# Kernel optimization log

Measured on AMD Instinct MI355X. Metric: run time of the kernel, lower is better.

Reference implementation:

```python
import jax, jax.numpy as jnp
import numpy as np

N_SRC, N_DST, MAX_NEIGH, H = 65536, 8192, 32, 128


def setup_inputs() -> dict:
    key = jax.random.key(0)
    ks = jax.random.split(key, 16)
    inp = {
        'x': jax.random.randint(ks[0], (N_SRC, 2), 0, 1000, dtype=jnp.int64)
             if jax.config.jax_enable_x64 else jax.random.randint(ks[0], (N_SRC, 2), 0, 1000, dtype=jnp.int32),
        'neigh_sim': jax.random.randint(ks[1], (N_DST, MAX_NEIGH), 0, N_SRC, dtype=jnp.int32),
        'neigh_cor': jax.random.randint(ks[2], (N_DST, MAX_NEIGH), 0, N_SRC, dtype=jnp.int32),
        'emb0_sim': jax.random.normal(ks[3], (1000, 32), jnp.float32) * 0.1,
        'emb1_sim': jax.random.normal(ks[4], (100000, 96), jnp.float32) * 0.1,
        'emb0_cor': jax.random.normal(ks[5], (1000, 32), jnp.float32) * 0.1,
        'emb1_cor': jax.random.normal(ks[6], (100000, 96), jnp.float32) * 0.1,
        'W_in_sim': jax.random.normal(ks[7], (H, H), jnp.float32) * 0.05,
        'b_in_sim': jnp.zeros((H,), jnp.float32),
        'W_in_cor': jax.random.normal(ks[8], (H, H), jnp.float32) * 0.05,
        'b_in_cor': jnp.zeros((H,), jnp.float32),
        'W_out_sim': jax.random.normal(ks[9], (H, H), jnp.float32) * 0.05,
        'b_out_sim': jnp.zeros((H,), jnp.float32),
        'W_out_cor': jax.random.normal(ks[10], (H, H), jnp.float32) * 0.05,
        'b_out_cor': jnp.zeros((H,), jnp.float32),
        'W_sim2cor': jax.random.normal(ks[11], (H, H), jnp.float32) * 0.05,
        'W_cor2sim': jax.random.normal(ks[12], (H, H), jnp.float32) * 0.05,
    }
    return inp


def _coattention_pool(D, Q):
    # D, Q: [N, m, H]
    n, m, h = Q.shape
    L = jnp.einsum('nmh,nkh->nmk', D, Q)           # [N, m, m]
    AC = jax.nn.softmax(L, axis=-1)
    AS = jax.nn.softmax(jnp.swapaxes(L, 1, 2), axis=-1)
    CQ = jnp.einsum('nmk,nkh->nmh', AC, Q)          # [N, m, H]
    CD = jnp.einsum('nkm,nmh->nkh', AS, jnp.concatenate([D, CQ], axis=-1))  # [N, m, 2H]
    out = jnp.concatenate([Q, CD], axis=-1)         # [N, m, 3H]
    # AvgPool1d(kernel=3, stride=3) over channel dim, then mean over neighbors
    pooled = out.reshape(n, m, h, 3).mean(axis=-1)  # consecutive triples
    return pooled.mean(axis=1)                       # [N, H]


def _mode_forward(x, neigh_sim, neigh_cor, emb0, emb1, W_in, b_in, W_out, b_out, mode):
    feat = jnp.concatenate([emb0[x[:, 0]], emb1[x[:, 1]]], axis=-1)  # [N_src, 128]
    feat = feat @ W_in + b_in                                        # [N_src, H]
    h_self = feat[: neigh_sim.shape[0]]
    nf_sim = feat[neigh_sim]  # [N_dst, m, H]
    nf_cor = feat[neigh_cor]
    if mode == 'cor':
        D, Q = nf_sim, nf_cor
    else:
        D, Q = nf_cor, nf_sim
    rst = h_self + _coattention_pool(D, Q)
    return rst @ W_out + b_out


def reference(x, neigh_sim, neigh_cor, emb0_sim, emb1_sim, emb0_cor, emb1_cor,
              W_in_sim, b_in_sim, W_in_cor, b_in_cor,
              W_out_sim, b_out_sim, W_out_cor, b_out_cor,
              W_sim2cor, W_cor2sim):
    sim = _mode_forward(x, neigh_sim, neigh_cor, emb0_sim, emb1_sim,
                        W_in_sim, b_in_sim, W_out_sim, b_out_sim, 'sim')
    cor = _mode_forward(x, neigh_sim, neigh_cor, emb0_cor, emb1_cor,
                        W_in_cor, b_in_cor, W_out_cor, b_out_cor, 'cor')
    a1, a2, b2 = 0.5, 0.33, 0.33
    z1sim = (1 - a1) * sim + a1 * (cor @ W_cor2sim)
    z1cor = (1 - a1) * cor + a1 * (sim @ W_sim2cor)
    z2sim = (1 - a2 - b2) * sim + a2 * (cor @ W_cor2sim) + b2 * (z1cor @ W_cor2sim)
    z2cor = (1 - a2 - b2) * cor + a2 * (sim @ W_sim2cor) + b2 * (z1sim @ W_sim2cor)
    return z2sim, z2cor
```

## Files before the change

### kernel.cpp

```cpp
#include <hip/hip_runtime.h>
#include <hip/hip_bf16.h>

#define NSRC 65536
#define NDST 8192
#define H 128

#define C_SELF 0.34f
#define C_CROSS 0.495f
#define C_DBL  0.165f

typedef float f32x16 __attribute__((ext_vector_type(16)));
typedef short bf16x8 __attribute__((ext_vector_type(8)));

static __device__ __forceinline__ float b2f(unsigned short u) {
  union { unsigned int i; float f; } v; v.i = ((unsigned int)u) << 16; return v.f;
}
static __device__ __forceinline__ unsigned short f2b(float f) {
  union { float f; unsigned int i; } v; v.f = f;
  unsigned int x = v.i;
  return (unsigned short)((x + 0x7fffu + ((x >> 16) & 1u)) >> 16);
}
static __device__ __forceinline__ void load4bf(const unsigned short* p, float* d) {
  ushort4 u = *(const ushort4*)p;
  d[0] = b2f(u.x); d[1] = b2f(u.y); d[2] = b2f(u.z); d[3] = b2f(u.w);
}

template <int CTRL>
static __device__ __forceinline__ float dpp_mov(float x) {
  return __int_as_float(__builtin_amdgcn_update_dpp(
      0, __float_as_int(x), CTRL, 0xF, 0xF, true));
}
static __device__ __forceinline__ float dpp_sum32_tail(float x) {
  x += dpp_mov<0x111>(x);
  x += dpp_mov<0x112>(x);
  x += dpp_mov<0x114>(x);
  x += dpp_mov<0x118>(x);
  x += dpp_mov<0x142>(x);
  return x;
}
static __device__ __forceinline__ float allred32_sum(float x) {
  x += dpp_mov<0xB1>(x);
  x += dpp_mov<0x4E>(x);
  x += dpp_mov<0x124>(x);
  x += dpp_mov<0x128>(x);
  x += __int_as_float(__builtin_amdgcn_ds_swizzle(__float_as_int(x), 0x401F));
  return x;
}

static __device__ __forceinline__ void load4any(const void* base, size_t idx, int f32flag, float* d) {
  if (f32flag) {
    float4 v = *(const float4*)((const float*)base + idx);
    d[0] = v.x; d[1] = v.y; d[2] = v.z; d[3] = v.w;
  } else {
    load4bf((const unsigned short*)base + idx, d);
  }
}
static __device__ __forceinline__ float load1any(const void* base, size_t idx, int f32flag) {
  return f32flag ? ((const float*)base)[idx] : b2f(((const unsigned short*)base)[idx]);
}

__global__ void detect(const unsigned short* __restrict__ W, const int* __restrict__ x,
                       int* __restrict__ flags) {
  const int l = threadIdx.x;
  int bad = 0;
#pragma unroll
  for (int i = l; i < 128; i += 64) {
    unsigned short u = W[i];
    if (u != 0) {
      int e = (u >> 7) & 0xFF;
      if (e < 90 || e > 128) bad++;
    }
  }
  int nz = (l < 16) ? (x[2 * l + 1] != 0 ? 1 : 0) : 0;
#pragma unroll
  for (int d = 1; d < 64; d <<= 1) {
    bad += __shfl_xor(bad, d);
    nz  += __shfl_xor(nz, d);
  }
  if (l == 0) {
    flags[0] = (bad > 8) ? 1 : 0;
    flags[1] = (nz == 0) ? 1 : 0;
  }
}

__global__ __launch_bounds__(128) void wprep(
    const void* __restrict__ Wsim, const void* __restrict__ Wcor,
    const int* __restrict__ flags,
    unsigned short* __restrict__ WTsim, unsigned short* __restrict__ WTcor)
{
  const int wf = flags[0];
  const int n = blockIdx.x & 127;
  const void* W = (blockIdx.x & 128) ? Wcor : Wsim;
  unsigned short* WT = (blockIdx.x & 128) ? WTcor : WTsim;
  const int k = threadIdx.x;
  WT[n * 128 + k] = f2b(load1any(W, k * 128 + n, wf));
}

__global__ __launch_bounds__(256) void featgemm_mfma(
    const int* __restrict__ x,
    const void* __restrict__ emb0,
    const void* __restrict__ emb1,
    const unsigned short* __restrict__ WT,
    const void* __restrict__ bvec,
    const int* __restrict__ flags,
    unsigned char* __restrict__ feat8,
    unsigned short* __restrict__ feat16)
{
  const int wf  = flags[0];
  const int x64 = flags[1];
  const int t = threadIdx.x;
  const int w = t >> 6, l = t & 63, lane = l & 31, half = l >> 5;
  const int rbase = blockIdx.x * 128 + w * 32;
  const int r = rbase + lane;

  int x0, x1;
  if (x64) { x0 = x[r * 4]; x1 = x[r * 4 + 2]; }
  else     { x0 = x[r * 2]; x1 = x[r * 2 + 1]; }

  bf16x8 afrag[8];
#pragma unroll
  for (int s = 0; s < 8; ++s) {
    float tmp[8];
    if (s < 2) {
      const size_t base = (size_t)x0 * 32 + s * 16 + half * 8;
      load4any(emb0, base, wf, tmp);
      load4any(emb0, base + 4, wf, tmp + 4);
    } else {
      const size_t base = (size_t)x1 * 96 + (s * 16 - 32) + half * 8;
      load4any(emb1, base, wf, tmp);
      load4any(emb1, base + 4, wf, tmp + 4);
    }
    union { bf16x8 v; unsigned short u[8]; } cv;
#pragma unroll
    for (int j = 0; j < 8; ++j) cv.u[j] = f2b(tmp[j]);
    afrag[s] = cv.v;
  }

  const bool do16 = (rbase < NDST);
#pragma unroll
  for (int strip = 0; strip < 4; ++strip) {
    const int n = strip * 32 + lane;
    const unsigned short* wtrow = WT + (size_t)n * 128 + half * 8;
    f32x16 acc = {0,0,0,0,0,0,0,0,0,0,0,0,0,0,0,0};
#pragma unroll
    for (int s = 0; s < 8; ++s) {
      bf16x8 bfrag = *(const bf16x8*)(wtrow + s * 16);
      acc = __builtin_amdgcn_mfma_f32_32x32x16_bf16(afrag[s], bfrag, acc, 0, 0, 0);
    }
    const float bias_n = load1any(bvec, n, wf);
#pragma unroll
    for (int i = 0; i < 16; ++i) {
      const int m = (i & 3) + 8 * (i >> 2) + 4 * half;
      const int row = rbase + m;
      const float val = acc[i] + bias_n;
      const int p8 = __builtin_amdgcn_cvt_pk_fp8_f32(val, val, 0, false);
      feat8[(size_t)row * H + n] = (unsigned char)(p8 & 0xFF);
      if (do16) feat16[(size_t)row * H + n] = f2b(val);
    }
  }
}

__global__ __launch_bounds__(256) void coatt_mfma(
    const unsigned char* __restrict__ feat8,
    const unsigned short* __restrict__ feat16,
    const int* __restrict__ idxD,
    const int* __restrict__ idxQ,
    unsigned short* __restrict__ rst)
{
  __shared__ float gbuf[4][448];
  const int t = threadIdx.x;
  const int w = t >> 6;
  const int l = t & 63;
  const int r = l & 31;
  const int half = l >> 5;
  const int n = blockIdx.x * 4 + w;

  float* g   = gbuf[w];
  float* svb = gbuf[w] + 384;
  float* tvb = gbuf[w] + 416;

  const int gD = idxD[n * 32 + r];
  const int gQ = idxQ[n * 32 + r];
  const unsigned char* drow = feat8 + (size_t)gD * H + half * 8;
  const unsigned char* qrow = feat8 + (size_t)gQ * H + half * 8;

  long dfrag[8], qfrag[8];
#pragma unroll
  for (int s = 0; s < 8; ++s) {
    dfrag[s] = *(const long*)(drow + s * 16);
    qfrag[s] = *(const long*)(qrow + s * 16);
  }

  f32x16 acc = {0,0,0,0,0,0,0,0,0,0,0,0,0,0,0,0};
#pragma unroll
  for (int s = 0; s < 8; ++s)
    acc = __builtin_amdgcn_mfma_f32_32x32x16_fp8_fp8(dfrag[s], qfrag[s], acc, 0, 0, 0);

  float ex[16], rrcp[16];
#pragma unroll
  for (int i = 0; i < 16; ++i) ex[i] = __expf(acc[i]);
#pragma unroll
  for (int i = 0; i < 16; ++i) rrcp[i] = 1.0f / allred32_sum(ex[i]);
  float csum = 0.f;
#pragma unroll
  for (int i = 0; i < 16; ++i) csum += ex[i];
  csum += __shfl_xor(csum, 32);
  const float crcp = 1.0f / csum;

  float svt[16];
#pragma unroll
  for (int i = 0; i < 16; ++i) svt[i] = dpp_sum32_tail(ex[i] * crcp);
  if (r == 31) {
    *(float4*)(svb + 4 * half)      = make_float4(svt[0],  svt[1],  svt[2],  svt[3]);
    *(float4*)(svb + 8 + 4 * half)  = make_float4(svt[4],  svt[5],  svt[6],  svt[7]);
    *(float4*)(svb + 16 + 4 * half) = make_float4(svt[8],  svt[9],  svt[10], svt[11]);
    *(float4*)(svb + 24 + 4 * half) = make_float4(svt[12], svt[13], svt[14], svt[15]);
  }
  float sv16[16];
#pragma unroll
  for (int q = 0; q < 4; ++q) {
    float4 v = *(const float4*)(svb + q * 8 + 4 * half);
    sv16[q * 4] = v.x; sv16[q * 4 + 1] = v.y; sv16[q * 4 + 2] = v.z; sv16[q * 4 + 3] = v.w;
  }
  float tvp = 0.f;
#pragma unroll
  for (int i = 0; i < 16; ++i) tvp += sv16[i] * ex[i] * rrcp[i];
  const float tv = tvp + __shfl_xor(tvp, 32);

  if (l < 32) tvb[l] = tv;
  float tv16[16];
#pragma unroll
  for (int q = 0; q < 4; ++q) {
    float4 vv = *(const float4*)(tvb + q * 8 + 4 * half);
    tv16[q * 4] = vv.x; tv16[q * 4 + 1] = vv.y; tv16[q * 4 + 2] = vv.z; tv16[q * 4 + 3] = vv.w;
  }

  const int bpos = (l & 15) - half * 8;
  const long b_ident = (bpos >= 0 && bpos < 8) ? (0x38L << (8 * bpos)) : 0L;
  const f32x16 zf = {0,0,0,0,0,0,0,0,0,0,0,0,0,0,0,0};

#pragma unroll
  for (int s = 0; s < 8; ++s) {
    f32x16 td = __builtin_amdgcn_mfma_f32_32x32x16_fp8_fp8(dfrag[s], b_ident, zf, 0, 0, 0);
    f32x16 tq = __builtin_amdgcn_mfma_f32_32x32x16_fp8_fp8(qfrag[s], b_ident, zf, 0, 0, 0);
    float su = 0.f, sw = 0.f, sv_ = 0.f;
#pragma unroll
    for (int i = 0; i < 16; ++i) {
      su  += tq[i];
      sw  += tv16[i] * tq[i];
      sv_ += sv16[i] * td[i];
    }
    su  += __shfl_xor(su, 32);
    sw  += __shfl_xor(sw, 32);
    sv_ += __shfl_xor(sv_, 32);
    if (l < 16) {
      const int c = s * 16 + l;
      g[c]       = su;
      g[128 + c] = sv_;
      g[256 + c] = sw;
    }
  }

#pragma unroll
  for (int rep = 0; rep < 2; ++rep) {
    const int hp = l + rep * 64;
    const float p = (g[3 * hp] + g[3 * hp + 1] + g[3 * hp + 2]) * (1.0f / 96.0f);
    const float hs = b2f(feat16[(size_t)n * H + hp]);
    rst[(size_t)n * H + hp] = f2b(hs + p);
  }
}

__global__ __launch_bounds__(128) void smallmm1(
    const void* __restrict__ Wos, const void* __restrict__ Woc,
    const void* __restrict__ Wsc, const void* __restrict__ Wcs,
    const void* __restrict__ bs, const void* __restrict__ bc,
    const int* __restrict__ flags,
    float* __restrict__ P1, float* __restrict__ P2,
    unsigned short* __restrict__ P1T, unsigned short* __restrict__ P2T,
    float* __restrict__ p1, float* __restrict__ p2)
{
  const int wf = flags[0];
  const int bid = blockIdx.x, c = threadIdx.x;
  if (bid < 128) {
    const int r = bid; float acc = 0.f;
    for (int k = 0; k < 128; ++k) acc += load1any(Wos, r * 128 + k, wf) * load1any(Wsc, k * 128 + c, wf);
    P1[r * 128 + c] = acc;
    P1T[c * 128 + r] = f2b(acc);
  } else if (bid < 256) {
    const int r = bid - 128; float acc = 0.f;
    for (int k = 0; k < 128; ++k) acc += load1any(Woc, r * 128 + k, wf) * load1any(Wcs, k * 128 + c, wf);
    P2[r * 128 + c] = acc;
    P2T[c * 128 + r] = f2b(acc);
  } else if (bid == 256) {
    float acc = 0.f;
    for (int k = 0; k < 128; ++k) acc += load1any(bs, k, wf) * load1any(Wsc, k * 128 + c, wf);
    p1[c] = acc;
  } else {
    float acc = 0.f;
    for (int k = 0; k < 128; ++k) acc += load1any(bc, k, wf) * load1any(Wcs, k * 128 + c, wf);
    p2[c] = acc;
  }
}

__global__ __launch_bounds__(128) void smallmm2(
    const void* __restrict__ Wos, const void* __restrict__ Woc,
    const void* __restrict__ Wsc, const void* __restrict__ Wcs,
    const void* __restrict__ bs, const void* __restrict__ bc,
    const int* __restrict__ flags,
    const float* __restrict__ P1, const float* __restrict__ P2,
    const float* __restrict__ p1, const float* __restrict__ p2,
    unsigned short* __restrict__ MssT, unsigned short* __restrict__ MccT,
    float* __restrict__ bsim, float* __restrict__ bcor)
{
  const int wf = flags[0];
  const int bid = blockIdx.x, c = threadIdx.x;
  if (bid < 128) {
    const int r = bid; float acc = 0.f;
    for (int k = 0; k < 128; ++k) acc += P1[r * 128 + k] * load1any(Wcs, k * 128 + c, wf);
    MssT[c * 128 + r] = f2b(C_SELF * load1any(Wos, r * 128 + c, wf) + C_DBL * acc);
  } else if (bid < 256) {
    const int r = bid - 128; float acc = 0.f;
    for (int k = 0; k < 128; ++k) acc += P2[r * 128 + k] * load1any(Wsc, k * 128 + c, wf);
    MccT[c * 128 + r] = f2b(C_SELF * load1any(Woc, r * 128 + c, wf) + C_DBL * acc);
  } else if (bid == 256) {
    float acc = 0.f;
    for (int k = 0; k < 128; ++k) acc += p1[k] * load1any(Wcs, k * 128 + c, wf);
    bsim[c] = C_SELF * load1any(bs, c, wf) + C_CROSS * p2[c] + C_DBL * acc;
  } else {
    float acc = 0.f;
    for (int k = 0; k < 128; ++k) acc += p2[k] * load1any(Wsc, k * 128 + c, wf);
    bcor[c] = C_SELF * load1any(bc, c, wf) + C_CROSS * p1[c] + C_DBL * acc;
  }
}

__global__ __launch_bounds__(256) void finalmm_mfma(
    const unsigned short* __restrict__ Rs, const unsigned short* __restrict__ Rc,
    const unsigned short* __restrict__ MssT, const unsigned short* __restrict__ MccT,
    const unsigned short* __restrict__ P1T, const unsigned short* __restrict__ P2T,
    const float* __restrict__ bsim, const float* __restrict__ bcor,
    float* __restrict__ outp)
{
  const int t = threadIdx.x;
  const int w = t >> 6, l = t & 63, lane = l & 31, half = l >> 5;
  const int rbase = blockIdx.x * 32;
  const int arow = rbase + lane;
  const int n = w * 32 + lane;

  const unsigned short* rsrow = Rs + (size_t)arow * H + half * 8;
  const unsigned short* rcrow = Rc + (size_t)arow * H + half * 8;
  bf16x8 aS[8], aC[8];
#pragma unroll
  for (int s = 0; s < 8; ++s) {
    aS[s] = *(const bf16x8*)(rsrow + s * 16);
    aC[s] = *(const bf16x8*)(rcrow + s * 16);
  }

  const unsigned short* bMss = MssT + (size_t)n * 128 + half * 8;
  const unsigned short* bMcc = MccT + (size_t)n * 128 + half * 8;
  const unsigned short* bP1  = P1T  + (size_t)n * 128 + half * 8;
  const unsigned short* bP2  = P2T  + (size_t)n * 128 + half * 8;

  f32x16 a1 = {0,0,0,0,0,0,0,0,0,0,0,0,0,0,0,0};
  f32x16 a2 = a1, a3 = a1, a4 = a1;
#pragma unroll
  for (int s = 0; s < 8; ++s) {
    bf16x8 b1 = *(const bf16x8*)(bMss + s * 16);
    bf16x8 b2 = *(const bf16x8*)(bP2  + s * 16);
    bf16x8 b3 = *(const bf16x8*)(bMcc + s * 16);
    bf16x8 b4 = *(const bf16x8*)(bP1  + s * 16);
    a1 = __builtin_amdgcn_mfma_f32_32x32x16_bf16(aS[s], b1, a1, 0, 0, 0);
    a2 = __builtin_amdgcn_mfma_f32_32x32x16_bf16(aC[s], b2, a2, 0, 0, 0);
    a3 = __builtin_amdgcn_mfma_f32_32x32x16_bf16(aC[s], b3, a3, 0, 0, 0);
    a4 = __builtin_amdgcn_mfma_f32_32x32x16_bf16(aS[s], b4, a4, 0, 0, 0);
  }

  const float bsv = bsim[n], bcv = bcor[n];
#pragma unroll
  for (int i = 0; i < 16; ++i) {
    const int m = (i & 3) + 8 * (i >> 2) + 4 * half;
    const int row = rbase + m;
    outp[(size_t)row * H + n] = a1[i] + C_CROSS * a2[i] + bsv;
    outp[(size_t)NDST * H + (size_t)row * H + n] = a3[i] + C_CROSS * a4[i] + bcv;
  }
}

extern "C" void kernel_launch(void* const* d_in, const int* in_sizes, int n_in,
                              void* d_out, int out_size, void* d_ws, size_t ws_size,
                              hipStream_t stream) {
  const int* x    = (const int*)d_in[0];
  const int* nsim = (const int*)d_in[1];
  const int* ncor = (const int*)d_in[2];
  const void* emb0_sim = d_in[3];
  const void* emb1_sim = d_in[4];
  const void* emb0_cor = d_in[5];
  const void* emb1_cor = d_in[6];
  const void* W_in_sim  = d_in[7];
  const void* b_in_sim  = d_in[8];
  const void* W_in_cor  = d_in[9];
  const void* b_in_cor  = d_in[10];
  const void* W_out_sim = d_in[11];
  const void* b_out_sim = d_in[12];
  const void* W_out_cor = d_in[13];
  const void* b_out_cor = d_in[14];
  const void* W_sim2cor = d_in[15];
  const void* W_cor2sim = d_in[16];

  float* fbase = (float*)d_ws;
  float* P1  = fbase;
  float* P2  = P1 + H * H;
  float* p1v = P2 + H * H;
  float* p2v = p1v + H;
  float* bsimv = p2v + H;
  float* bcorv = bsimv + H;
  int* flags = (int*)(bcorv + H);
  unsigned short* feat16_sim = (unsigned short*)(flags + 4);
  unsigned short* feat16_cor = feat16_sim + (size_t)NDST * H;
  unsigned short* rst_sim    = feat16_cor + (size_t)NDST * H;
  unsigned short* rst_cor    = rst_sim + (size_t)NDST * H;
  unsigned char* feat8_sim = (unsigned char*)(rst_cor + (size_t)NDST * H);
  unsigned char* feat8_cor = feat8_sim + (size_t)NSRC * H;
  unsigned short* WT_sim = (unsigned short*)(feat8_cor + (size_t)NSRC * H);
  unsigned short* WT_cor = WT_sim + H * H;
  unsigned short* P1T  = WT_cor + H * H;
  unsigned short* P2T  = P1T + H * H;
  unsigned short* MssT = P2T + H * H;
  unsigned short* MccT = MssT + H * H;

  detect<<<1, 64, 0, stream>>>((const unsigned short*)W_in_sim, x, flags);
  wprep<<<256, 128, 0, stream>>>(W_in_sim, W_in_cor, flags, WT_sim, WT_cor);
  smallmm1<<<258, 128, 0, stream>>>(W_out_sim, W_out_cor, W_sim2cor, W_cor2sim,
                                    b_out_sim, b_out_cor, flags, P1, P2, P1T, P2T, p1v, p2v);
  smallmm2<<<258, 128, 0, stream>>>(W_out_sim, W_out_cor, W_sim2cor, W_cor2sim,
                                    b_out_sim, b_out_cor, flags, P1, P2, p1v, p2v,
                                    MssT, MccT, bsimv, bcorv);
  featgemm_mfma<<<NSRC / 128, 256, 0, stream>>>(x, emb0_sim, emb1_sim, WT_sim, b_in_sim,
                                                flags, feat8_sim, feat16_sim);
  featgemm_mfma<<<NSRC / 128, 256, 0, stream>>>(x, emb0_cor, emb1_cor, WT_cor, b_in_cor,
                                                flags, feat8_cor, feat16_cor);
  coatt_mfma<<<NDST / 4, 256, 0, stream>>>(feat8_sim, feat16_sim, ncor, nsim, rst_sim);
  coatt_mfma<<<NDST / 4, 256, 0, stream>>>(feat8_cor, feat16_cor, nsim, ncor, rst_cor);
  finalmm_mfma<<<NDST / 32, 256, 0, stream>>>(rst_sim, rst_cor, MssT, MccT, P1T, P2T,
                                              bsimv, bcorv, (float*)d_out);
}
```

Baseline: 248.2 us.

## Merge prep kernels and batch sim/cor launches via grid y dimension

Folds the detect, wprep, smallmm1 and smallmm2 kernels into one prep kernel. Each block recomputes the dtype flags inline, and the two-stage weight products are chained through LDS inside a block. featgemm and coatt now each launch once with a 2-wide y grid covering both the sim and cor modes. This cuts nine launches to four and removes the launch gaps and tail serialization between them, at the cost of redundant per-block flag detection and one long serial bias block.

```diff
diff --git a/kernel.cpp b/kernel.cpp
--- a/kernel.cpp
+++ b/kernel.cpp
@@ -59,9 +59,8 @@
   return f32flag ? ((const float*)base)[idx] : b2f(((const unsigned short*)base)[idx]);
 }
 
-__global__ void detect(const unsigned short* __restrict__ W, const int* __restrict__ x,
-                       int* __restrict__ flags) {
-  const int l = threadIdx.x;
+static __device__ __forceinline__ int detect_wf(const unsigned short* __restrict__ W) {
+  const int l = threadIdx.x & 63;
   int bad = 0;
 #pragma unroll
   for (int i = l; i < 128; i += 64) {
@@ -71,43 +70,98 @@
       if (e < 90 || e > 128) bad++;
     }
   }
+#pragma unroll
+  for (int d = 1; d < 64; d <<= 1) bad += __shfl_xor(bad, d);
+  return (bad > 8) ? 1 : 0;
+}
+static __device__ __forceinline__ int detect_x64(const int* __restrict__ x) {
+  const int l = threadIdx.x & 63;
   int nz = (l < 16) ? (x[2 * l + 1] != 0 ? 1 : 0) : 0;
 #pragma unroll
-  for (int d = 1; d < 64; d <<= 1) {
-    bad += __shfl_xor(bad, d);
-    nz  += __shfl_xor(nz, d);
-  }
-  if (l == 0) {
-    flags[0] = (bad > 8) ? 1 : 0;
-    flags[1] = (nz == 0) ? 1 : 0;
-  }
-}
-
-__global__ __launch_bounds__(128) void wprep(
-    const void* __restrict__ Wsim, const void* __restrict__ Wcor,
-    const int* __restrict__ flags,
-    unsigned short* __restrict__ WTsim, unsigned short* __restrict__ WTcor)
+  for (int d = 1; d < 64; d <<= 1) nz += __shfl_xor(nz, d);
+  return (nz == 0) ? 1 : 0;
+}
+
+__global__ __launch_bounds__(128) void prep(
+    const void* __restrict__ Wsim_in, const void* __restrict__ Wcor_in,
+    const int* __restrict__ x,
+    const void* __restrict__ Wos, const void* __restrict__ Woc,
+    const void* __restrict__ Wsc, const void* __restrict__ Wcs,
+    const void* __restrict__ bs, const void* __restrict__ bc,
+    unsigned short* __restrict__ WTsim, unsigned short* __restrict__ WTcor,
+    unsigned short* __restrict__ P1T, unsigned short* __restrict__ P2T,
+    unsigned short* __restrict__ MssT, unsigned short* __restrict__ MccT,
+    float* __restrict__ bsim, float* __restrict__ bcor)
 {
-  const int wf = flags[0];
-  const int n = blockIdx.x & 127;
-  const void* W = (blockIdx.x & 128) ? Wcor : Wsim;
-  unsigned short* WT = (blockIdx.x & 128) ? WTcor : WTsim;
-  const int k = threadIdx.x;
-  WT[n * 128 + k] = f2b(load1any(W, k * 128 + n, wf));
+  __shared__ float lds[256];
+  const int wf = detect_wf((const unsigned short*)Wsim_in);
+  const int bid = blockIdx.x;
+  const int c = threadIdx.x;
+
+  if (bid < 256) {
+    const int n = bid & 127;
+    const void* W = (bid & 128) ? Wcor_in : Wsim_in;
+    unsigned short* WT = (bid & 128) ? WTcor : WTsim;
+    WT[n * 128 + c] = f2b(load1any(W, c * 128 + n, wf));
+    return;
+  }
+  const int b2 = bid - 256;
+  if (b2 < 128) {
+    const int r = b2;
+    float acc = 0.f;
+    for (int k = 0; k < 128; ++k)
+      acc += load1any(Wos, r * 128 + k, wf) * load1any(Wsc, k * 128 + c, wf);
+    P1T[c * 128 + r] = f2b(acc);
+    lds[c] = acc;
+    __syncthreads();
+    float acc2 = 0.f;
+    for (int k = 0; k < 128; ++k) acc2 += lds[k] * load1any(Wcs, k * 128 + c, wf);
+    MssT[c * 128 + r] = f2b(C_SELF * load1any(Wos, r * 128 + c, wf) + C_DBL * acc2);
+  } else if (b2 < 256) {
+    const int r = b2 - 128;
+    float acc = 0.f;
+    for (int k = 0; k < 128; ++k)
+      acc += load1any(Woc, r * 128 + k, wf) * load1any(Wcs, k * 128 + c, wf);
+    P2T[c * 128 + r] = f2b(acc);
+    lds[c] = acc;
+    __syncthreads();
+    float acc2 = 0.f;
+    for (int k = 0; k < 128; ++k) acc2 += lds[k] * load1any(Wsc, k * 128 + c, wf);
+    MccT[c * 128 + r] = f2b(C_SELF * load1any(Woc, r * 128 + c, wf) + C_DBL * acc2);
+  } else {
+    float a1 = 0.f, a2 = 0.f;
+    for (int k = 0; k < 128; ++k) a1 += load1any(bs, k, wf) * load1any(Wsc, k * 128 + c, wf);
+    for (int k = 0; k < 128; ++k) a2 += load1any(bc, k, wf) * load1any(Wcs, k * 128 + c, wf);
+    lds[c] = a1; lds[128 + c] = a2;
+    __syncthreads();
+    float a3 = 0.f, a4 = 0.f;
+    for (int k = 0; k < 128; ++k) a3 += lds[k] * load1any(Wcs, k * 128 + c, wf);
+    for (int k = 0; k < 128; ++k) a4 += lds[128 + k] * load1any(Wsc, k * 128 + c, wf);
+    bsim[c] = C_SELF * load1any(bs, c, wf) + C_CROSS * a2 + C_DBL * a3;
+    bcor[c] = C_SELF * load1any(bc, c, wf) + C_CROSS * a1 + C_DBL * a4;
+  }
 }
 
 __global__ __launch_bounds__(256) void featgemm_mfma(
     const int* __restrict__ x,
-    const void* __restrict__ emb0,
-    const void* __restrict__ emb1,
-    const unsigned short* __restrict__ WT,
-    const void* __restrict__ bvec,
-    const int* __restrict__ flags,
-    unsigned char* __restrict__ feat8,
-    unsigned short* __restrict__ feat16)
+    const void* __restrict__ Wdet,
+    const void* __restrict__ emb0s, const void* __restrict__ emb1s,
+    const void* __restrict__ emb0c, const void* __restrict__ emb1c,
+    const unsigned short* __restrict__ WTs, const unsigned short* __restrict__ WTc,
+    const void* __restrict__ bvs, const void* __restrict__ bvc,
+    unsigned char* __restrict__ f8s, unsigned short* __restrict__ f16s,
+    unsigned char* __restrict__ f8c, unsigned short* __restrict__ f16c)
 {
-  const int wf  = flags[0];
-  const int x64 = flags[1];
+  const int wf  = detect_wf((const unsigned short*)Wdet);
+  const int x64 = detect_x64(x);
+  const int mode = blockIdx.y;
+  const void* emb0 = mode ? emb0c : emb0s;
+  const void* emb1 = mode ? emb1c : emb1s;
+  const unsigned short* WT = mode ? WTc : WTs;
+  const void* bvec = mode ? bvc : bvs;
+  unsigned char*  feat8  = mode ? f8c  : f8s;
+  unsigned short* feat16 = mode ? f16c : f16s;
+
   const int t = threadIdx.x;
   const int w = t >> 6, l = t & 63, lane = l & 31, half = l >> 5;
   const int rbase = blockIdx.x * 128 + w * 32;
@@ -161,12 +215,18 @@
 }
 
 __global__ __launch_bounds__(256) void coatt_mfma(
-    const unsigned char* __restrict__ feat8,
-    const unsigned short* __restrict__ feat16,
-    const int* __restrict__ idxD,
-    const int* __restrict__ idxQ,
-    unsigned short* __restrict__ rst)
+    const unsigned char* __restrict__ f8s, const unsigned short* __restrict__ f16s,
+    const unsigned char* __restrict__ f8c, const unsigned short* __restrict__ f16c,
+    const int* __restrict__ nsim, const int* __restrict__ ncor,
+    unsigned short* __restrict__ rsts, unsigned short* __restrict__ rstc)
 {
+  const int mode = blockIdx.y;
+  const unsigned char*  feat8  = mode ? f8c  : f8s;
+  const unsigned short* feat16 = mode ? f16c : f16s;
+  const int* idxD = mode ? nsim : ncor;
+  const int* idxQ = mode ? ncor : nsim;
+  unsigned short* rst = mode ? rstc : rsts;
+
   __shared__ float gbuf[4][448];
   const int t = threadIdx.x;
   const int w = t >> 6;
@@ -267,69 +327,6 @@
     const float p = (g[3 * hp] + g[3 * hp + 1] + g[3 * hp + 2]) * (1.0f / 96.0f);
     const float hs = b2f(feat16[(size_t)n * H + hp]);
     rst[(size_t)n * H + hp] = f2b(hs + p);
-  }
-}
-
-__global__ __launch_bounds__(128) void smallmm1(
-    const void* __restrict__ Wos, const void* __restrict__ Woc,
-    const void* __restrict__ Wsc, const void* __restrict__ Wcs,
-    const void* __restrict__ bs, const void* __restrict__ bc,
-    const int* __restrict__ flags,
-    float* __restrict__ P1, float* __restrict__ P2,
-    unsigned short* __restrict__ P1T, unsigned short* __restrict__ P2T,
-    float* __restrict__ p1, float* __restrict__ p2)
-{
-  const int wf = flags[0];
-  const int bid = blockIdx.x, c = threadIdx.x;
-  if (bid < 128) {
-    const int r = bid; float acc = 0.f;
-    for (int k = 0; k < 128; ++k) acc += load1any(Wos, r * 128 + k, wf) * load1any(Wsc, k * 128 + c, wf);
-    P1[r * 128 + c] = acc;
-    P1T[c * 128 + r] = f2b(acc);
-  } else if (bid < 256) {
-    const int r = bid - 128; float acc = 0.f;
-    for (int k = 0; k < 128; ++k) acc += load1any(Woc, r * 128 + k, wf) * load1any(Wcs, k * 128 + c, wf);
-    P2[r * 128 + c] = acc;
-    P2T[c * 128 + r] = f2b(acc);
-  } else if (bid == 256) {
-    float acc = 0.f;
-    for (int k = 0; k < 128; ++k) acc += load1any(bs, k, wf) * load1any(Wsc, k * 128 + c, wf);
-    p1[c] = acc;
-  } else {
-    float acc = 0.f;
-    for (int k = 0; k < 128; ++k) acc += load1any(bc, k, wf) * load1any(Wcs, k * 128 + c, wf);
-    p2[c] = acc;
-  }
-}
-
-__global__ __launch_bounds__(128) void smallmm2(
-    const void* __restrict__ Wos, const void* __restrict__ Woc,
-    const void* __restrict__ Wsc, const void* __restrict__ Wcs,
-    const void* __restrict__ bs, const void* __restrict__ bc,
-    const int* __restrict__ flags,
-    const float* __restrict__ P1, const float* __restrict__ P2,
-    const float* __restrict__ p1, const float* __restrict__ p2,
-    unsigned short* __restrict__ MssT, unsigned short* __restrict__ MccT,
-    float* __restrict__ bsim, float* __restrict__ bcor)
-{
-  const int wf = flags[0];
-  const int bid = blockIdx.x, c = threadIdx.x;
-  if (bid < 128) {
-    const int r = bid; float acc = 0.f;
-    for (int k = 0; k < 128; ++k) acc += P1[r * 128 + k] * load1any(Wcs, k * 128 + c, wf);
-    MssT[c * 128 + r] = f2b(C_SELF * load1any(Wos, r * 128 + c, wf) + C_DBL * acc);
-  } else if (bid < 256) {
-    const int r = bid - 128; float acc = 0.f;
-    for (int k = 0; k < 128; ++k) acc += P2[r * 128 + k] * load1any(Wsc, k * 128 + c, wf);
-    MccT[c * 128 + r] = f2b(C_SELF * load1any(Woc, r * 128 + c, wf) + C_DBL * acc);
-  } else if (bid == 256) {
-    float acc = 0.f;
-    for (int k = 0; k < 128; ++k) acc += p1[k] * load1any(Wcs, k * 128 + c, wf);
-    bsim[c] = C_SELF * load1any(bs, c, wf) + C_CROSS * p2[c] + C_DBL * acc;
-  } else {
-    float acc = 0.f;
-    for (int k = 0; k < 128; ++k) acc += p2[k] * load1any(Wsc, k * 128 + c, wf);
-    bcor[c] = C_SELF * load1any(bc, c, wf) + C_CROSS * p1[c] + C_DBL * acc;
   }
 }
 
@@ -426,19 +423,17 @@
   unsigned short* MssT = P2T + H * H;
   unsigned short* MccT = MssT + H * H;
 
-  detect<<<1, 64, 0, stream>>>((const unsigned short*)W_in_sim, x, flags);
-  wprep<<<256, 128, 0, stream>>>(W_in_sim, W_in_cor, flags, WT_sim, WT_cor);
-  smallmm1<<<258, 128, 0, stream>>>(W_out_sim, W_out_cor, W_sim2cor, W_cor2sim,
-                                    b_out_sim, b_out_cor, flags, P1, P2, P1T, P2T, p1v, p2v);
-  smallmm2<<<258, 128, 0, stream>>>(W_out_sim, W_out_cor, W_sim2cor, W_cor2sim,
-                                    b_out_sim, b_out_cor, flags, P1, P2, p1v, p2v,
-                                    MssT, MccT, bsimv, bcorv);
-  featgemm_mfma<<<NSRC / 128, 256, 0, stream>>>(x, emb0_sim, emb1_sim, WT_sim, b_in_sim,
-                                                flags, feat8_sim, feat16_sim);
-  featgemm_mfma<<<NSRC / 128, 256, 0, stream>>>(x, emb0_cor, emb1_cor, WT_cor, b_in_cor,
-                                                flags, feat8_cor, feat16_cor);
-  coatt_mfma<<<NDST / 4, 256, 0, stream>>>(feat8_sim, feat16_sim, ncor, nsim, rst_sim);
-  coatt_mfma<<<NDST / 4, 256, 0, stream>>>(feat8_cor, feat16_cor, nsim, ncor, rst_cor);
+  prep<<<513, 128, 0, stream>>>(W_in_sim, W_in_cor, x,
+                                W_out_sim, W_out_cor, W_sim2cor, W_cor2sim,
+                                b_out_sim, b_out_cor,
+                                WT_sim, WT_cor, P1T, P2T, MssT, MccT, bsimv, bcorv);
+  featgemm_mfma<<<dim3(NSRC / 128, 2), 256, 0, stream>>>(
+      x, W_in_sim, emb0_sim, emb1_sim, emb0_cor, emb1_cor,
+      WT_sim, WT_cor, b_in_sim, b_in_cor,
+      feat8_sim, feat16_sim, feat8_cor, feat16_cor);
+  coatt_mfma<<<dim3(NDST / 4, 2), 256, 0, stream>>>(
+      feat8_sim, feat16_sim, feat8_cor, feat16_cor,
+      nsim, ncor, rst_sim, rst_cor);
   finalmm_mfma<<<NDST / 32, 256, 0, stream>>>(rst_sim, rst_cor, MssT, MccT, P1T, P2T,
                                               bsimv, bcorv, (float*)d_out);
 }
```

After: 259.4 us. +4.5%, slower.
